# Optimization experiments

Measured on AMD Instinct MI355X. Metric: run time of the kernel, lower is better.

The kernel has to match this reference:

```python
import jax, jax.numpy as jnp
import numpy as np

DIM = 192; HEADS = 6; WS = 8; SHIFT = 4; HID = int(DIM * 4.0)
CAB_SCALE = 0.01; COMPRESS = 3; SQUEEZE = 30
B = 8; H0 = 128; W0 = 128


def window_partition(x, ws):
    Bn, H, W, C = x.shape
    x = x.reshape(Bn, H // ws, ws, W // ws, ws, C).transpose(0, 1, 3, 2, 4, 5)
    return x.reshape(-1, ws, ws, C)


def window_reverse(w, ws, H, W):
    Bn = w.shape[0] // ((H // ws) * (W // ws))
    x = w.reshape(Bn, H // ws, W // ws, ws, ws, -1).transpose(0, 1, 3, 2, 4, 5)
    return x.reshape(Bn, H, W, -1)


def layernorm(x, w, b):
    mu = jnp.mean(x, -1, keepdims=True)
    var = jnp.var(x, -1, keepdims=True)
    return (x - mu) * jax.lax.rsqrt(var + 1e-5) * w + b


def conv3x3(x, w, b):
    y = jax.lax.conv_general_dilated(x, w, (1, 1), [(1, 1), (1, 1)],
                                     dimension_numbers=('NCHW', 'OIHW', 'NCHW'))
    return y + b[None, :, None, None]


def _coords_table(ws):
    # continuous relative coords table, log-spaced as in SwinV2
    r = np.arange(-(ws - 1), ws, dtype=np.float32)
    t = np.stack(np.meshgrid(r, r, indexing='ij'), -1) / (ws - 1) * 8.0
    t = np.sign(t) * np.log2(np.abs(t) + 1.0) / np.log2(8.0)
    return jnp.asarray(t.reshape(-1, 2))  # ((2ws-1)^2, 2)


def _rel_index(ws):
    c = np.stack(np.meshgrid(np.arange(ws), np.arange(ws), indexing='ij')).reshape(2, -1)
    r = (c[:, :, None] - c[:, None, :]).transpose(1, 2, 0)
    r[..., 0] += ws - 1; r[..., 1] += ws - 1; r[..., 0] *= 2 * ws - 1
    return jnp.asarray(r.sum(-1))  # (N, N) int


def _attn_mask(H, W, ws, shift):
    img = np.zeros((1, H, W, 1), np.float32); cnt = 0
    for hs in (slice(0, -ws), slice(-ws, -shift), slice(-shift, None)):
        for wsl in (slice(0, -ws), slice(-ws, -shift), slice(-shift, None)):
            img[:, hs, wsl, :] = cnt; cnt += 1
    win = img.reshape(1, H // ws, ws, W // ws, ws, 1).transpose(0, 1, 3, 2, 4, 5).reshape(-1, ws * ws)
    m = win[:, None, :] - win[:, :, None]
    return jnp.asarray(np.where(m != 0, -100.0, 0.0).astype(np.float32))  # (nW, N, N)


def _forward(x, norm1_w, norm1_b, qkv_w, q_bias, v_bias, logit_scale,
             cpb_w1, cpb_b1, cpb_w2, proj_w, proj_b,
             cab1_w, cab1_b, cab2_w, cab2_b, ca1_w, ca1_b, ca2_w, ca2_b,
             norm2_w, norm2_b, fc1_w, fc1_b, fc2_w, fc2_b, H, W):
    Bn, L, C = x.shape
    nh = HEADS; hd = C // nh; N = WS * WS
    shortcut = x
    xn = layernorm(x, norm1_w, norm1_b)
    xi = xn.reshape(Bn, H, W, C)

    # ---- CAB branch (Conv-GELU-Conv + channel attention) ----
    xc = xi.transpose(0, 3, 1, 2)                      # NCHW
    c = conv3x3(xc, cab1_w, cab1_b)
    c = jax.nn.gelu(c, approximate=False)
    c = conv3x3(c, cab2_w, cab2_b)
    s = c.mean((2, 3))                                 # (B, C) squeeze
    s = jax.nn.relu(s @ ca1_w.T + ca1_b)
    s = jax.nn.sigmoid(s @ ca2_w.T + ca2_b)
    conv_x = (c * s[:, :, None, None]).transpose(0, 2, 3, 1).reshape(Bn, L, C)

    # ---- shifted-window cosine attention ----
    xs = jnp.roll(xi, (-SHIFT, -SHIFT), axis=(1, 2)) if SHIFT > 0 else xi
    xw = window_partition(xs, WS).reshape(-1, N, C)    # (B*nW, N, C)
    qkv_bias = jnp.concatenate([q_bias, jnp.zeros_like(v_bias), v_bias])
    qkv = (xw @ qkv_w.T + qkv_bias).reshape(-1, N, 3, nh, hd).transpose(2, 0, 3, 1, 4)
    q, k, v = qkv[0], qkv[1], qkv[2]                   # (B_, nh, N, hd)
    qn = q / jnp.maximum(jnp.linalg.norm(q, axis=-1, keepdims=True), 1e-12)
    kn = k / jnp.maximum(jnp.linalg.norm(k, axis=-1, keepdims=True), 1e-12)
    attn = jnp.einsum('bhnd,bhmd->bhnm', qn, kn)
    scale = jnp.exp(jnp.minimum(logit_scale, jnp.log(100.0)))  # (nh,1,1)
    attn = attn * scale
    # CPB MLP relative position bias
    hbias = jax.nn.relu(_coords_table(WS) @ cpb_w1.T + cpb_b1) @ cpb_w2.T  # (T, nh)
    rpb = hbias[_rel_index(WS).reshape(-1)].reshape(N, N, nh).transpose(2, 0, 1)
    attn = attn + 16.0 * jax.nn.sigmoid(rpb)[None]
    if SHIFT > 0:
        mask = _attn_mask(H, W, WS, SHIFT)             # (nW, N, N)
        nW = mask.shape[0]
        attn = (attn.reshape(-1, nW, nh, N, N) + mask[None, :, None]).reshape(-1, nh, N, N)
    attn = jax.nn.softmax(attn, axis=-1)
    out = jnp.einsum('bhnm,bhmd->bhnd', attn, v).transpose(0, 2, 1, 3).reshape(-1, N, C)
    out = out @ proj_w.T + proj_b
    out = window_reverse(out.reshape(-1, WS, WS, C), WS, H, W)
    if SHIFT > 0:
        out = jnp.roll(out, (SHIFT, SHIFT), axis=(1, 2))
    attn_x = out.reshape(Bn, L, C)

    x = shortcut + attn_x + CAB_SCALE * conv_x
    h = layernorm(x, norm2_w, norm2_b)
    h = jax.nn.gelu(h @ fc1_w.T + fc1_b, approximate=False) @ fc2_w.T + fc2_b
    return x + h


def setup_inputs() -> dict:
    key = jax.random.key(0)
    ks = jax.random.split(key, 24)
    r = lambda k, shp, s=0.02: (jax.random.normal(k, shp, jnp.float32) * s)
    C = DIM; Cc = DIM // COMPRESS; Cs = DIM // SQUEEZE
    return {
        'x': jax.random.normal(ks[0], (B, H0 * W0, C), jnp.float32),
        'H': H0, 'W': W0,
        'norm1_w': jnp.ones((C,), jnp.float32), 'norm1_b': jnp.zeros((C,), jnp.float32),
        'qkv_w': r(ks[1], (3 * C, C)),
        'q_bias': jnp.zeros((C,), jnp.float32), 'v_bias': jnp.zeros((C,), jnp.float32),
        'logit_scale': jnp.full((HEADS, 1, 1), np.log(10.0), jnp.float32),
        'cpb_w1': r(ks[2], (512, 2), 0.1), 'cpb_b1': jnp.zeros((512,), jnp.float32),
        'cpb_w2': r(ks[3], (HEADS, 512), 0.1),
        'proj_w': r(ks[4], (C, C)), 'proj_b': jnp.zeros((C,), jnp.float32),
        'cab1_w': r(ks[5], (Cc, C, 3, 3)), 'cab1_b': jnp.zeros((Cc,), jnp.float32),
        'cab2_w': r(ks[6], (C, Cc, 3, 3)), 'cab2_b': jnp.zeros((C,), jnp.float32),
        'ca1_w': r(ks[7], (Cs, C)), 'ca1_b': jnp.zeros((Cs,), jnp.float32),
        'ca2_w': r(ks[8], (C, Cs)), 'ca2_b': jnp.zeros((C,), jnp.float32),
        'norm2_w': jnp.ones((C,), jnp.float32), 'norm2_b': jnp.zeros((C,), jnp.float32),
        'fc1_w': r(ks[9], (HID, C)), 'fc1_b': jnp.zeros((HID,), jnp.float32),
        'fc2_w': r(ks[10], (C, HID)), 'fc2_b': jnp.zeros((C,), jnp.float32),
    }


def reference(x, H, W, norm1_w, norm1_b, qkv_w, q_bias, v_bias, logit_scale,
              cpb_w1, cpb_b1, cpb_w2, proj_w, proj_b,
              cab1_w, cab1_b, cab2_w, cab2_b, ca1_w, ca1_b, ca2_w, ca2_b,
              norm2_w, norm2_b, fc1_w, fc1_b, fc2_w, fc2_b):
    return _forward(x, norm1_w, norm1_b, qkv_w, q_bias, v_bias, logit_scale,
                    cpb_w1, cpb_b1, cpb_w2, proj_w, proj_b,
                    cab1_w, cab1_b, cab2_w, cab2_b, ca1_w, ca1_b, ca2_w, ca2_b,
                    norm2_w, norm2_b, fc1_w, fc1_b, fc2_w, fc2_b, int(H), int(W))
```

## Files before the change

kernel.cpp:

```cpp
#include <hip/hip_runtime.h>
#include <math.h>


typedef unsigned short u16;
typedef __attribute__((ext_vector_type(8))) short short8;
typedef __attribute__((ext_vector_type(4))) float f32x4;

#define DI static __device__ __forceinline__

DI float b2f(u16 u){ union{unsigned u; float f;} v; v.u = ((unsigned)u)<<16; return v.f; }
DI u16 f2b(float f){ union{float f; unsigned u;} v; v.f = f; unsigned r = v.u + 0x7fffu + ((v.u>>16)&1u); return (u16)(r>>16); }
DI float gelu_f(float x){ return 0.5f*x*(1.0f+erff(x*0.7071067811865475f)); }

#define L_TOK 131072
#define C2PLANE (12582912L)

__global__ __launch_bounds__(256) void ln_k(const float* __restrict__ in,
    const float* __restrict__ w, const float* __restrict__ b, u16* __restrict__ out)
{
  const int row  = blockIdx.x*4 + (threadIdx.x>>6);
  const int lane = threadIdx.x & 63;
  const float* r = in + (long)row*192;
  float v0 = r[lane], v1 = r[lane+64], v2 = r[lane+128];
  float s = v0+v1+v2;
  #pragma unroll
  for (int m=1;m<64;m<<=1) s += __shfl_xor(s, m);
  float mu = s*(1.0f/192.0f);
  float d0=v0-mu, d1=v1-mu, d2=v2-mu;
  float q = d0*d0+d1*d1+d2*d2;
  #pragma unroll
  for (int m=1;m<64;m<<=1) q += __shfl_xor(q, m);
  float rstd = rsqrtf(q*(1.0f/192.0f)+1e-5f);
  u16* o = out + (long)row*192;
  o[lane]     = f2b(d0*rstd*w[lane]    +b[lane]);
  o[lane+64]  = f2b(d1*rstd*w[lane+64] +b[lane+64]);
  o[lane+128] = f2b(d2*rstd*w[lane+128]+b[lane+128]);
}

__global__ __launch_bounds__(256) void prep_k(
    const float* __restrict__ qkv_w, const float* __restrict__ q_bias,
    const float* __restrict__ v_bias, const float* __restrict__ proj_w,
    const float* __restrict__ fc1_w, const float* __restrict__ fc2_w,
    const float* __restrict__ cab1_w, const float* __restrict__ cab2_w,
    const float* __restrict__ lgs,
    float* __restrict__ qkvbias, u16* __restrict__ wqkv, u16* __restrict__ wproj,
    u16* __restrict__ wfc1, u16* __restrict__ wfc2, u16* __restrict__ wt1,
    u16* __restrict__ wt2, float* __restrict__ scale6)
{
  int o = blockIdx.x*256 + threadIdx.x;
  if (o < 576){ qkvbias[o] = (o<192)? q_bias[o] : ((o<384)? 0.f : v_bias[o-384]); return; }
  o -= 576;
  if (o < 110592){ wqkv[o] = f2b(qkv_w[o]); return; } o -= 110592;
  if (o < 36864){ wproj[o] = f2b(proj_w[o]); return; } o -= 36864;
  if (o < 147456){ wfc1[o] = f2b(fc1_w[o]); return; } o -= 147456;
  if (o < 147456){ wfc2[o] = f2b(fc2_w[o]); return; } o -= 147456;
  if (o < 110592){
    int s = o/12288, r = o%12288, oc = r/192, ic = r%192, kh = s/3, kw = s%3;
    wt1[o] = f2b(cab1_w[((oc*192+ic)*3+kh)*3+kw]); return; } o -= 110592;
  if (o < 110592){
    int s = o/12288, r = o%12288, oc = r/64, ic = r%64, kh = s/3, kw = s%3;
    wt2[o] = f2b(cab2_w[((oc*64+ic)*3+kh)*3+kw]); return; } o -= 110592;
  if (o < 6){ scale6[o] = expf(fminf(lgs[o], logf(100.f))); }
}

__global__ __launch_bounds__(256) void rpb_k(const float* __restrict__ w1,
    const float* __restrict__ b1, const float* __restrict__ w2, float* __restrict__ rpbL)
{
  __shared__ float hb[225*6];
  const int tid = threadIdx.x;
  if (tid < 225){
    int di = tid/15, dj = tid%15;
    float vi = (di-7)*(8.0f/7.0f), vj = (dj-7)*(8.0f/7.0f);
    float t0 = (vi==0.f)?0.f:copysignf(log2f(fabsf(vi)+1.f)*(1.f/3.f), vi);
    float t1 = (vj==0.f)?0.f:copysignf(log2f(fabsf(vj)+1.f)*(1.f/3.f), vj);
    float acc[6] = {0,0,0,0,0,0};
    for (int hd=0; hd<512; ++hd){
      float a = fmaxf(t0*w1[hd*2] + t1*w1[hd*2+1] + b1[hd], 0.f);
      #pragma unroll
      for (int h=0;h<6;++h) acc[h] += a*w2[h*512+hd];
    }
    #pragma unroll
    for (int h=0;h<6;++h) hb[tid*6+h] = acc[h];
  }
  __syncthreads();
  for (int o = tid; o < 24576; o += 256){
    int i = o&3, lane = (o>>2)&63, mK = (o>>8)&3, nQ = (o>>10)&3, h = o>>12;
    int q = nQ*16 + (lane&15), k = mK*16 + (lane>>4)*4 + i;
    int idx = ((q>>3)-(k>>3)+7)*15 + ((q&7)-(k&7)+7);
    rpbL[o] = 16.0f/(1.0f+expf(-hb[idx*6+h]));
  }
}

template<int EPI, int KK, int NN>
__global__ __launch_bounds__(256) void gemm4_k(
    const u16* __restrict__ A, const u16* __restrict__ W,
    const float* __restrict__ bias, const float* __restrict__ resx,
    const u16* __restrict__ c2in, const float* __restrict__ sgate,
    float* __restrict__ outf, u16* __restrict__ outb)
{
  constexpr int KC = KK/192;
  constexpr int NP = NN/64;
  __shared__ __align__(16) u16 As[128*200];
  __shared__ __align__(16) u16 Bs[64*200];
  const int tid = threadIdx.x, w = tid>>6, lane = tid&63;
  const int fr = lane&15, g = lane>>4;
  const int m0 = blockIdx.x*128;
  u16*   obuf = Bs;
  float* fbuf = (float*)Bs;

  #define STAGE_A(kc) { \
    _Pragma("unroll") \
    for (int i=0;i<12;++i){ const int id=tid+i*256, row=id/24, cc=id%24; \
      *(short8*)&As[row*200+cc*8] = \
        *(const short8*)(A + (long)(m0+row)*KK + (kc)*192 + cc*8); } }
  #define KLOOP(accr) { \
    _Pragma("unroll") \
    for (int ks=0; ks<6; ++ks){ \
      short8 af0 = *(const short8*)&As[(w*32+     fr)*200 + ks*32 + g*8]; \
      short8 af1 = *(const short8*)&As[(w*32+16+  fr)*200 + ks*32 + g*8]; \
      _Pragma("unroll") \
      for (int nr=0;nr<4;++nr){ \
        short8 bf = *(const short8*)&Bs[(nr*16+fr)*200 + ks*32 + g*8]; \
        accr[0][nr] = __builtin_amdgcn_mfma_f32_16x16x32_bf16(af0, bf, accr[0][nr], 0,0,0); \
        accr[1][nr] = __builtin_amdgcn_mfma_f32_16x16x32_bf16(af1, bf, accr[1][nr], 0,0,0); \
      } } }

  #define EPI_BF16(accr, n0) { \
    __syncthreads(); \
    _Pragma("unroll") \
    for (int mr=0;mr<2;++mr) \
      _Pragma("unroll") \
      for (int nr=0;nr<4;++nr){ \
        const float bc = bias[(n0)+nr*16+fr]; \
        _Pragma("unroll") \
        for (int i=0;i<4;++i){ \
          const int tok = w*32+mr*16+g*4+i; \
          float v = accr[mr][nr][i] + bc; \
          if (EPI==4) v = gelu_f(v); \
          obuf[tok*72 + nr*16+fr] = f2b(v); } } \
    __syncthreads(); \
    _Pragma("unroll") \
    for (int j=0;j<4;++j){ \
      const int idx = tid + j*256, tok = idx>>3, cc = idx&7; \
      *(short8*)(outb + (long)(m0+tok)*NN + (n0) + cc*8) = \
          *(const short8*)&obuf[tok*72 + cc*8]; } }

  #define EPI_F32(accr, n0) { \
    _Pragma("unroll") \
    for (int h=0;h<2;++h){ \
      __syncthreads(); \
      if ((w>>1)==h){ \
        _Pragma("unroll") \
        for (int mr=0;mr<2;++mr) \
          _Pragma("unroll") \
          for (int nr=0;nr<4;++nr){ \
            const float bc = bias[(n0)+nr*16+fr]; \
            _Pragma("unroll") \
            for (int i=0;i<4;++i){ \
              const int tok = (w&1)*32+mr*16+g*4+i; \
              fbuf[tok*68 + nr*16+fr] = accr[mr][nr][i] + bc; } } } \
      __syncthreads(); \
      _Pragma("unroll") \
      for (int j=0;j<4;++j){ \
        const int idx = tid + j*256, t = idx>>4, cc = idx&15; \
        const int tokg = m0 + h*64 + t, gc0 = (n0) + cc*4; \
        f32x4 v = *(const f32x4*)&fbuf[t*68 + cc*4]; \
        const long o = (long)tokg*NN + gc0; \
        if constexpr (EPI==3){ \
          const f32x4 r = *(const f32x4*)(resx + o); \
          const int pl = (gc0>=96); \
          const u16* cp = c2in + (long)pl*C2PLANE + (long)tokg*96 + (gc0 - pl*96); \
          const float* sg = sgate + (tokg>>14)*192 + gc0; \
          _Pragma("unroll") \
          for (int e=0;e<4;++e) v[e] += r[e] + 0.01f*b2f(cp[e])*sg[e]; \
        } else { \
          const f32x4 r = *(const f32x4*)(outf + o); \
          _Pragma("unroll") \
          for (int e=0;e<4;++e) v[e] += r[e]; \
        } \
        *(f32x4*)(outf + o) = v; } } }

  short8 breg[6];
  #define LOADB(p) { \
    _Pragma("unroll") \
    for (int i=0;i<6;++i){ const int id=tid+i*256, br=id/24, cc=id%24; \
      breg[i] = *(const short8*)(W + (long)((p)*64+br)*KK + cc*8); } }
  #define STOREB() { \
    _Pragma("unroll") \
    for (int i=0;i<6;++i){ const int id=tid+i*256, br=id/24, cc=id%24; \
      *(short8*)&Bs[br*200+cc*8] = breg[i]; } }

  if constexpr (KC == 1){
    STAGE_A(0);
    LOADB(0);
    for (int p=0; p<NP; ++p){
      __syncthreads();
      STOREB();
      __syncthreads();
      if (p+1 < NP) LOADB(p+1);
      f32x4 acc[2][4];
      #pragma unroll
      for (int a=0;a<2;++a)
        #pragma unroll
        for (int b=0;b<4;++b) acc[a][b] = (f32x4){0.f,0.f,0.f,0.f};
      KLOOP(acc);
      if constexpr (EPI==0 || EPI==4){ EPI_BF16(acc, p*64); }
      else                           { EPI_F32(acc, p*64); }
    }
  } else {
    f32x4 acc[NP][2][4];
    #pragma unroll
    for (int p=0;p<NP;++p)
      #pragma unroll
      for (int a=0;a<2;++a)
        #pragma unroll
        for (int b=0;b<4;++b) acc[p][a][b] = (f32x4){0.f,0.f,0.f,0.f};
    for (int kc=0; kc<KC; ++kc){
      __syncthreads();
      STAGE_A(kc);
      #pragma unroll
      for (int p=0;p<NP;++p){
        __syncthreads();
        #pragma unroll
        for (int i=0;i<6;++i){ const int id=tid+i*256, br=id/24, cc=id%24;
          *(short8*)&Bs[br*200+cc*8] =
            *(const short8*)(W + (long)(p*64+br)*KK + kc*192 + cc*8); }
        __syncthreads();
        KLOOP(acc[p]);
      }
    }
    #pragma unroll
    for (int p=0;p<NP;++p){ EPI_F32(acc[p], p*64); }
  }
  #undef STAGE_A
  #undef KLOOP
  #undef EPI_BF16
  #undef EPI_F32
  #undef LOADB
  #undef STOREB
}

template<int EPI, int CG, int IC, int OCT, int OCP, int NR, int TG>
__global__ __launch_bounds__(256, 2) void conv4_k(
    const u16* __restrict__ A, const u16* __restrict__ Wt,
    const float* __restrict__ bias, u16* __restrict__ outb,
    float* __restrict__ ssum)
{
  constexpr int NTG = 9/TG, S = CG*NTG;
  constexpr int WN = (TG*OCP*4 + 255)/256;
  __shared__ __align__(16) u16 Ah[4*130*36];
  __shared__ __align__(16) u16 Wl[TG*OCP*36];
  const int tid = threadIdx.x, w = tid>>6, lane = tid&63;
  const int fr = lane&15, g = lane>>4;
  const int b = blockIdx.x>>6, y0 = (blockIdx.x&63)*2;
  const int oc0 = blockIdx.y*OCP;
  const int wrow = w>>1, wcol = (w&1)*64;

  f32x4 acc[4][NR];
  #pragma unroll
  for (int a=0;a<4;++a)
    #pragma unroll
    for (int n=0;n<NR;++n) acc[a][n] = (f32x4){0.f,0.f,0.f,0.f};

  short8 hreg[8], wreg[WN];

  #define PRELOAD(s) { \
    const int cg_=(s)/NTG, tg_=(s)%NTG; \
    if (tg_==0){ \
      _Pragma("unroll") \
      for (int i=0;i<8;++i){ \
        const int id=tid+i*256, p=id>>9, x=(id>>2)&127, cc=id&3, y=y0+p-1; \
        short8 v={0,0,0,0,0,0,0,0}; \
        if ((unsigned)y<128u) \
          v = *(const short8*)(A + (long)((((b<<7)|y)<<7)|x)*IC + cg_*32 + cc*8); \
        hreg[i]=v; } } \
    _Pragma("unroll") \
    for (int i=0;i<WN;++i){ \
      const int id=tid+i*256; \
      if (id < TG*OCP*4){ \
        const int t=id/(OCP*4), r=id%(OCP*4), oc=r>>2, cc=r&3; \
        wreg[i] = *(const short8*)(Wt + \
            (long)((tg_*TG+t)*OCT + oc0 + oc)*IC + cg_*32 + cc*8); } } }

  #define STORE_STAGED(s) { \
    const int tg_=(s)%NTG; \
    if (tg_==0){ \
      _Pragma("unroll") \
      for (int i=0;i<8;++i){ \
        const int id=tid+i*256, p=id>>9, x=(id>>2)&127, cc=id&3; \
        *(short8*)&Ah[(p*130 + x + 1)*36 + cc*8] = hreg[i]; } \
      if (tid < 32){ \
        const int p=tid>>3, r=tid&7, col=(r>>2)?129:0, cc=r&3; \
        *(short8*)&Ah[(p*130 + col)*36 + cc*8] = (short8){0,0,0,0,0,0,0,0}; } } \
    _Pragma("unroll") \
    for (int i=0;i<WN;++i){ \
      const int id=tid+i*256; \
      if (id < TG*OCP*4){ \
        const int t=id/(OCP*4), r=id%(OCP*4), oc=r>>2, cc=r&3; \
        *(short8*)&Wl[(t*OCP+oc)*36 + cc*8] = wreg[i]; } } }

  #define COMPUTE(s) { \
    const int tg_=(s)%NTG; \
    _Pragma("unroll") \
    for (int t=0;t<TG;++t){ \
      const int tap=tg_*TG+t, dy=tap/3, dx=tap%3; \
      short8 bf[NR]; \
      _Pragma("unroll") \
      for (int nr=0;nr<NR;++nr) \
        bf[nr] = *(const short8*)&Wl[(t*OCP + nr*16 + fr)*36 + g*8]; \
      short8 af[4]; \
      _Pragma("unroll") \
      for (int mr=0;mr<4;++mr) \
        af[mr] = *(const short8*)&Ah[((wrow+dy)*130 + wcol + mr*16 + fr + dx)*36 + g*8]; \
      _Pragma("unroll") \
      for (int mr=0;mr<4;++mr) \
        _Pragma("unroll") \
        for (int nr=0;nr<NR;++nr) \
          acc[mr][nr] = __builtin_amdgcn_mfma_f32_16x16x32_bf16(af[mr], bf[nr], acc[mr][nr], 0,0,0); } }

  PRELOAD(0);
  for (int s=0; s<S; ++s){
    __syncthreads();
    STORE_STAGED(s);
    __syncthreads();
    if (s+1 < S) PRELOAD(s+1);
    COMPUTE(s);
  }
  #undef PRELOAD
  #undef STORE_STAGED
  #undef COMPUTE

  if constexpr (EPI==2){
    #pragma unroll
    for (int nr=0;nr<NR;++nr){
      const float bc = bias[oc0 + nr*16 + fr];
      float s = 0.f;
      #pragma unroll
      for (int mr=0;mr<4;++mr)
        #pragma unroll
        for (int i=0;i<4;++i) s += acc[mr][nr][i] + bc;
      s += __shfl_xor(s,16); s += __shfl_xor(s,32);
      if (lane < 16) atomicAdd(&ssum[b*192 + oc0 + nr*16 + lane], s);
    }
  }

  u16* ob = Ah;
  const long tb = (long)(((b<<7)|y0)<<7);
  __syncthreads();
  if constexpr (EPI==1){
    #pragma unroll
    for (int mr=0;mr<4;++mr)
      #pragma unroll
      for (int nr=0;nr<NR;++nr){
        const float bc = bias[nr*16 + fr];
        #pragma unroll
        for (int i=0;i<4;++i){
          const int tok = wrow*128 + wcol + mr*16 + g*4 + i;
          ob[tok*72 + nr*16+fr] = f2b(gelu_f(acc[mr][nr][i] + bc));
        }
      }
    __syncthreads();
    #pragma unroll
    for (int j=0;j<8;++j){
      const int idx = tid + j*256, tok = idx>>3, cc = idx&7;
      *(short8*)(outb + (tb+tok)*OCP + cc*8) = *(const short8*)&ob[tok*72 + cc*8];
    }
  } else {
    const long pbase = (long)blockIdx.y*C2PLANE;
    #pragma unroll
    for (int h=0;h<2;++h){
      if (h) __syncthreads();
      if (wrow == h){
        #pragma unroll
        for (int mr=0;mr<4;++mr)
          #pragma unroll
          for (int nr=0;nr<NR;++nr){
            const float bc = bias[oc0 + nr*16 + fr];
            #pragma unroll
            for (int i=0;i<4;++i){
              const int tok = wcol + mr*16 + g*4 + i;
              ob[tok*104 + nr*16+fr] = f2b(acc[mr][nr][i] + bc);
            }
          }
      }
      __syncthreads();
      #pragma unroll
      for (int j=0;j<6;++j){
        const int idx = tid + j*256, t = idx/12, cc = idx%12;
        *(short8*)(outb + pbase + (tb + h*128 + t)*96 + cc*8) =
            *(const short8*)&ob[t*104 + cc*8];
      }
    }
  }
}

__global__ __launch_bounds__(256) void se_k(const float* __restrict__ ssum,
    const float* __restrict__ ca1w, const float* __restrict__ ca1b,
    const float* __restrict__ ca2w, const float* __restrict__ ca2b,
    float* __restrict__ sgate)
{
  __shared__ float hid[48];
  const int tid = threadIdx.x;
  if (tid < 48){
    int b = tid/6, cs = tid%6;
    float a = ca1b[cs];
    for (int c=0;c<192;++c) a += ssum[b*192+c]*(1.f/16384.f)*ca1w[cs*192+c];
    hid[tid] = fmaxf(a, 0.f);
  }
  __syncthreads();
  for (int o = tid; o < 1536; o += 256){
    int b = o/192, c = o%192;
    float a = ca2b[c];
    #pragma unroll
    for (int cs=0;cs<6;++cs) a += hid[b*6+cs]*ca2w[c*6+cs];
    sgate[o] = 1.f/(1.f+expf(-a));
  }
}

__global__ __launch_bounds__(256) void attn_k(const u16* __restrict__ qkv,
    const float* __restrict__ rpbL, const float* __restrict__ scale6,
    u16* __restrict__ aout)
{
  __shared__ int  lidx_s[4][64];
  __shared__ char region_s[4][64];
  __shared__ __align__(16) u16 p_s[4][64*72];
  const int tid = threadIdx.x, w = tid>>6, lane = tid&63;
  const int task = blockIdx.x*4 + w;
  const int win = task/6, h = task - win*6;
  const int b = win>>8, wn = win&255, wy = wn>>4, wx = wn&15;
  {
    int i = lane>>3, j = lane&7;
    int hs = wy*8+i, ws = wx*8+j;
    lidx_s[w][lane] = (b<<14) | (((hs+4)&127)<<7) | ((ws+4)&127);
    int hb = hs<120?0:(hs<124?1:2), wb = ws<120?0:(ws<124?1:2);
    region_s[w][lane] = (char)(hb*3+wb);
  }
  __syncthreads();
  const int g = lane>>4, l15 = lane&15;
  const bool edge = (wy==15) || (wx==15);
  const float scl = scale6[h];
  const f32x4 zf = {0.f,0.f,0.f,0.f};

  short8 kf[4];
  #pragma unroll
  for (int mt=0; mt<4; ++mt){
    const long base = (long)lidx_s[w][mt*16+l15]*576 + 192 + h*32 + g*8;
    short8 r = *(const short8*)(qkv + base);
    float f[8]; float ss = 0.f;
    #pragma unroll
    for (int e=0;e<8;++e){ f[e] = b2f((u16)r[e]); ss += f[e]*f[e]; }
    ss += __shfl_xor(ss,16); ss += __shfl_xor(ss,32);
    const float inv = 1.0f/fmaxf(sqrtf(ss), 1e-12f);
    #pragma unroll
    for (int e=0;e<8;++e) kf[mt][e] = (short)f2b(f[e]*inv);
  }

  #pragma unroll
  for (int nt=0; nt<4; ++nt){
    short8 qf;
    {
      const long base = (long)lidx_s[w][nt*16+l15]*576 + h*32 + g*8;
      short8 r = *(const short8*)(qkv + base);
      float f[8]; float ss = 0.f;
      #pragma unroll
      for (int e=0;e<8;++e){ f[e] = b2f((u16)r[e]); ss += f[e]*f[e]; }
      ss += __shfl_xor(ss,16); ss += __shfl_xor(ss,32);
      const float inv = 1.0f/fmaxf(sqrtf(ss), 1e-12f);
      #pragma unroll
      for (int e=0;e<8;++e) qf[e] = (short)f2b(f[e]*inv);
    }
    f32x4 st[4];
    #pragma unroll
    for (int mt=0; mt<4; ++mt)
      st[mt] = __builtin_amdgcn_mfma_f32_16x16x32_bf16(kf[mt], qf, zf, 0, 0, 0);
    float lv[16];
    const float* rp = rpbL + ((h*4+nt)*4)*256 + lane*4;
    const int rq = edge ? region_s[w][nt*16+l15] : 0;
    #pragma unroll
    for (int mt=0; mt<4; ++mt){
      const f32x4 rb = *(const f32x4*)(rp + mt*256);
      #pragma unroll
      for (int i=0;i<4;++i){
        float v = st[mt][i]*scl + rb[i];
        if (edge && region_s[w][mt*16+g*4+i] != rq) v -= 100.0f;
        lv[mt*4+i] = v;
      }
    }
    float mx = lv[0];
    #pragma unroll
    for (int t=1;t<16;++t) mx = fmaxf(mx, lv[t]);
    mx = fmaxf(mx, __shfl_xor(mx,16)); mx = fmaxf(mx, __shfl_xor(mx,32));
    float sum = 0.f;
    #pragma unroll
    for (int t=0;t<16;++t){ lv[t] = __expf(lv[t]-mx); sum += lv[t]; }
    sum += __shfl_xor(sum,16); sum += __shfl_xor(sum,32);
    const float isum = 1.0f/sum;
    u16* pr = p_s[w] + (nt*16+l15)*72;
    #pragma unroll
    for (int mt=0; mt<4; ++mt){
      #pragma unroll
      for (int j=0;j<2;++j){
        unsigned lo = f2b(lv[mt*4+2*j]  *isum);
        unsigned hi = f2b(lv[mt*4+2*j+1]*isum);
        *(unsigned*)(pr + mt*16 + g*4 + 2*j) = lo | (hi<<16);
      }
    }
  }

  short8 vf[2][2];
  #pragma unroll
  for (int nd=0; nd<2; ++nd)
    #pragma unroll
    for (int kc=0; kc<2; ++kc)
      #pragma unroll
      for (int e=0;e<8;++e){
        const int tok = kc*32 + g*8 + e;
        vf[nd][kc][e] = (short)qkv[(long)lidx_s[w][tok]*576 + 384 + h*32 + nd*16 + l15];
      }

  __syncthreads();

  #pragma unroll
  for (int mt=0; mt<4; ++mt){
    const short8 a0 = *(const short8*)(p_s[w] + (mt*16+l15)*72 +      g*8);
    const short8 a1 = *(const short8*)(p_s[w] + (mt*16+l15)*72 + 32 + g*8);
    #pragma unroll
    for (int nd=0; nd<2; ++nd){
      f32x4 o = __builtin_amdgcn_mfma_f32_16x16x32_bf16(a0, vf[nd][0], zf, 0, 0, 0);
      o = __builtin_amdgcn_mfma_f32_16x16x32_bf16(a1, vf[nd][1], o, 0, 0, 0);
      #pragma unroll
      for (int i=0;i<4;++i){
        const int q = mt*16 + g*4 + i;
        aout[(long)lidx_s[w][q]*192 + h*32 + nd*16 + l15] = f2b(o[i]);
      }
    }
  }
}

extern "C" void kernel_launch(void* const* d_in, const int* in_sizes, int n_in,
                              void* d_out, int out_size, void* d_ws, size_t ws_size,
                              hipStream_t stream)
{
  const float* x     = (const float*)d_in[0];
  const float* n1w   = (const float*)d_in[3];
  const float* n1b   = (const float*)d_in[4];
  const float* qkvw  = (const float*)d_in[5];
  const float* qb    = (const float*)d_in[6];
  const float* vb    = (const float*)d_in[7];
  const float* lgs   = (const float*)d_in[8];
  const float* cpb1w = (const float*)d_in[9];
  const float* cpb1b = (const float*)d_in[10];
  const float* cpb2w = (const float*)d_in[11];
  const float* projw = (const float*)d_in[12];
  const float* projb = (const float*)d_in[13];
  const float* cab1w = (const float*)d_in[14];
  const float* cab1b = (const float*)d_in[15];
  const float* cab2w = (const float*)d_in[16];
  const float* cab2b = (const float*)d_in[17];
  const float* ca1w  = (const float*)d_in[18];
  const float* ca1b  = (const float*)d_in[19];
  const float* ca2w  = (const float*)d_in[20];
  const float* ca2b  = (const float*)d_in[21];
  const float* n2w   = (const float*)d_in[22];
  const float* n2b   = (const float*)d_in[23];
  const float* fc1w  = (const float*)d_in[24];
  const float* fc1b  = (const float*)d_in[25];
  const float* fc2w  = (const float*)d_in[26];
  const float* fc2b  = (const float*)d_in[27];
  float* dout = (float*)d_out;
  char* ws = (char*)d_ws;

  constexpr size_t OFF_XN  = 0;
  constexpr size_t OFF_G1  = 50331648;
  constexpr size_t OFF_C2  = 67108864;
  constexpr size_t OFF_AO  = 167772160;
  constexpr size_t OFF_QKV = 218103808;
  constexpr size_t OFF_X2N = OFF_QKV;
  constexpr size_t OFF_H1  = 0;
  constexpr size_t OFF_SM  = 369098752;

  u16*   xn      = (u16*)(ws + OFF_XN);
  u16*   g1      = (u16*)(ws + OFF_G1);
  u16*   c2      = (u16*)(ws + OFF_C2);
  u16*   ao      = (u16*)(ws + OFF_AO);
  u16*   qkvb    = (u16*)(ws + OFF_QKV);
  u16*   x2n     = (u16*)(ws + OFF_X2N);
  u16*   h1      = (u16*)(ws + OFF_H1);
  float* qkvbias = (float*)(ws + OFF_SM);
  float* scale6  = (float*)(ws + OFF_SM + 4096);
  float* ssum    = (float*)(ws + OFF_SM + 8192);
  float* sgate   = (float*)(ws + OFF_SM + 16384);
  float* rpbL    = (float*)(ws + OFF_SM + 24576);
  u16*   wqkv    = (u16*)(ws + OFF_SM + 131072);
  u16*   wproj   = (u16*)(ws + OFF_SM + 360448);
  u16*   wfc1    = (u16*)(ws + OFF_SM + 434176);
  u16*   wfc2    = (u16*)(ws + OFF_SM + 729088);
  u16*   wt1     = (u16*)(ws + OFF_SM + 1024000);
  u16*   wt2     = (u16*)(ws + OFF_SM + 1245184);

  prep_k<<<2595, 256, 0, stream>>>(qkvw, qb, vb, projw, fc1w, fc2w, cab1w, cab2w,
                                   lgs, qkvbias, wqkv, wproj, wfc1, wfc2, wt1, wt2, scale6);
  rpb_k<<<1, 256, 0, stream>>>(cpb1w, cpb1b, cpb2w, rpbL);
  ln_k<<<32768, 256, 0, stream>>>(x, n1w, n1b, xn);
  hipMemsetAsync(ssum, 0, 1536*4, stream);
  conv4_k<1,6,192,64,64,4,9><<<dim3(512,1), 256, 0, stream>>>(xn, wt1, cab1b, g1, nullptr);
  conv4_k<2,2,64,192,96,6,3><<<dim3(512,2), 256, 0, stream>>>(g1, wt2, cab2b, c2, ssum);
  se_k<<<1, 256, 0, stream>>>(ssum, ca1w, ca1b, ca2w, ca2b, sgate);
  gemm4_k<0,192,576><<<1024, 256, 0, stream>>>(xn, wqkv, qkvbias,
      nullptr, nullptr, nullptr, nullptr, qkvb);
  attn_k<<<3072, 256, 0, stream>>>(qkvb, rpbL, scale6, ao);
  gemm4_k<3,192,192><<<1024, 256, 0, stream>>>(ao, wproj, projb,
      x, c2, sgate, dout, nullptr);
  ln_k<<<32768, 256, 0, stream>>>(dout, n2w, n2b, x2n);
  gemm4_k<4,192,768><<<1024, 256, 0, stream>>>(x2n, wfc1, fc1b,
      nullptr, nullptr, nullptr, nullptr, h1);
  gemm4_k<5,768,192><<<1024, 256, 0, stream>>>(h1, wfc2, fc2b,
      nullptr, nullptr, nullptr, dout, nullptr);
}
```

Measured before the change: 715.6 us.

## Fuse LN2, fc1, GELU and fc2 into one MLP kernel; add dedicated proj kernel

The second LayerNorm, fc1 with GELU, and fc2 with the residual add now run in a single kernel per 64-token tile. The 768-wide hidden activation is staged in LDS chunk by chunk instead of being written to and read back from global memory, and the separate LN and GEMM launches go away. The projection GEMM gets its own 64-row kernel that reads weight fragments straight from global memory. The cost is fc2 weight fragments loaded from global (L2) on every chunk, and lower MFMA reuse per wave.

```diff
diff --git a/kernel.cpp b/kernel.cpp
--- a/kernel.cpp
+++ b/kernel.cpp
@@ -12,7 +12,6 @@
 DI u16 f2b(float f){ union{float f; unsigned u;} v; v.f = f; unsigned r = v.u + 0x7fffu + ((v.u>>16)&1u); return (u16)(r>>16); }
 DI float gelu_f(float x){ return 0.5f*x*(1.0f+erff(x*0.7071067811865475f)); }
 
-#define L_TOK 131072
 #define C2PLANE (12582912L)
 
 __global__ __launch_bounds__(256) void ln_k(const float* __restrict__ in,
@@ -94,91 +93,20 @@
 template<int EPI, int KK, int NN>
 __global__ __launch_bounds__(256) void gemm4_k(
     const u16* __restrict__ A, const u16* __restrict__ W,
-    const float* __restrict__ bias, const float* __restrict__ resx,
-    const u16* __restrict__ c2in, const float* __restrict__ sgate,
-    float* __restrict__ outf, u16* __restrict__ outb)
-{
-  constexpr int KC = KK/192;
+    const float* __restrict__ bias, u16* __restrict__ outb)
+{
   constexpr int NP = NN/64;
   __shared__ __align__(16) u16 As[128*200];
   __shared__ __align__(16) u16 Bs[64*200];
   const int tid = threadIdx.x, w = tid>>6, lane = tid&63;
   const int fr = lane&15, g = lane>>4;
   const int m0 = blockIdx.x*128;
-  u16*   obuf = Bs;
-  float* fbuf = (float*)Bs;
-
-  #define STAGE_A(kc) { \
-    _Pragma("unroll") \
-    for (int i=0;i<12;++i){ const int id=tid+i*256, row=id/24, cc=id%24; \
-      *(short8*)&As[row*200+cc*8] = \
-        *(const short8*)(A + (long)(m0+row)*KK + (kc)*192 + cc*8); } }
-  #define KLOOP(accr) { \
-    _Pragma("unroll") \
-    for (int ks=0; ks<6; ++ks){ \
-      short8 af0 = *(const short8*)&As[(w*32+     fr)*200 + ks*32 + g*8]; \
-      short8 af1 = *(const short8*)&As[(w*32+16+  fr)*200 + ks*32 + g*8]; \
-      _Pragma("unroll") \
-      for (int nr=0;nr<4;++nr){ \
-        short8 bf = *(const short8*)&Bs[(nr*16+fr)*200 + ks*32 + g*8]; \
-        accr[0][nr] = __builtin_amdgcn_mfma_f32_16x16x32_bf16(af0, bf, accr[0][nr], 0,0,0); \
-        accr[1][nr] = __builtin_amdgcn_mfma_f32_16x16x32_bf16(af1, bf, accr[1][nr], 0,0,0); \
-      } } }
-
-  #define EPI_BF16(accr, n0) { \
-    __syncthreads(); \
-    _Pragma("unroll") \
-    for (int mr=0;mr<2;++mr) \
-      _Pragma("unroll") \
-      for (int nr=0;nr<4;++nr){ \
-        const float bc = bias[(n0)+nr*16+fr]; \
-        _Pragma("unroll") \
-        for (int i=0;i<4;++i){ \
-          const int tok = w*32+mr*16+g*4+i; \
-          float v = accr[mr][nr][i] + bc; \
-          if (EPI==4) v = gelu_f(v); \
-          obuf[tok*72 + nr*16+fr] = f2b(v); } } \
-    __syncthreads(); \
-    _Pragma("unroll") \
-    for (int j=0;j<4;++j){ \
-      const int idx = tid + j*256, tok = idx>>3, cc = idx&7; \
-      *(short8*)(outb + (long)(m0+tok)*NN + (n0) + cc*8) = \
-          *(const short8*)&obuf[tok*72 + cc*8]; } }
-
-  #define EPI_F32(accr, n0) { \
-    _Pragma("unroll") \
-    for (int h=0;h<2;++h){ \
-      __syncthreads(); \
-      if ((w>>1)==h){ \
-        _Pragma("unroll") \
-        for (int mr=0;mr<2;++mr) \
-          _Pragma("unroll") \
-          for (int nr=0;nr<4;++nr){ \
-            const float bc = bias[(n0)+nr*16+fr]; \
-            _Pragma("unroll") \
-            for (int i=0;i<4;++i){ \
-              const int tok = (w&1)*32+mr*16+g*4+i; \
-              fbuf[tok*68 + nr*16+fr] = accr[mr][nr][i] + bc; } } } \
-      __syncthreads(); \
-      _Pragma("unroll") \
-      for (int j=0;j<4;++j){ \
-        const int idx = tid + j*256, t = idx>>4, cc = idx&15; \
-        const int tokg = m0 + h*64 + t, gc0 = (n0) + cc*4; \
-        f32x4 v = *(const f32x4*)&fbuf[t*68 + cc*4]; \
-        const long o = (long)tokg*NN + gc0; \
-        if constexpr (EPI==3){ \
-          const f32x4 r = *(const f32x4*)(resx + o); \
-          const int pl = (gc0>=96); \
-          const u16* cp = c2in + (long)pl*C2PLANE + (long)tokg*96 + (gc0 - pl*96); \
-          const float* sg = sgate + (tokg>>14)*192 + gc0; \
-          _Pragma("unroll") \
-          for (int e=0;e<4;++e) v[e] += r[e] + 0.01f*b2f(cp[e])*sg[e]; \
-        } else { \
-          const f32x4 r = *(const f32x4*)(outf + o); \
-          _Pragma("unroll") \
-          for (int e=0;e<4;++e) v[e] += r[e]; \
-        } \
-        *(f32x4*)(outf + o) = v; } } }
+  u16* obuf = Bs;
+
+  #pragma unroll
+  for (int i=0;i<12;++i){ const int id=tid+i*256, row=id/24, cc=id%24;
+    *(short8*)&As[row*200+cc*8] =
+      *(const short8*)(A + (long)(m0+row)*KK + cc*8); }
 
   short8 breg[6];
   #define LOADB(p) { \
@@ -190,54 +118,201 @@
     for (int i=0;i<6;++i){ const int id=tid+i*256, br=id/24, cc=id%24; \
       *(short8*)&Bs[br*200+cc*8] = breg[i]; } }
 
-  if constexpr (KC == 1){
-    STAGE_A(0);
-    LOADB(0);
-    for (int p=0; p<NP; ++p){
-      __syncthreads();
-      STOREB();
-      __syncthreads();
-      if (p+1 < NP) LOADB(p+1);
-      f32x4 acc[2][4];
-      #pragma unroll
-      for (int a=0;a<2;++a)
+  LOADB(0);
+  for (int p=0; p<NP; ++p){
+    __syncthreads();
+    STOREB();
+    __syncthreads();
+    if (p+1 < NP) LOADB(p+1);
+    f32x4 acc[2][4];
+    #pragma unroll
+    for (int a=0;a<2;++a)
+      #pragma unroll
+      for (int b=0;b<4;++b) acc[a][b] = (f32x4){0.f,0.f,0.f,0.f};
+    #pragma unroll
+    for (int ks=0; ks<6; ++ks){
+      short8 af0 = *(const short8*)&As[(w*32+   fr)*200 + ks*32 + g*8];
+      short8 af1 = *(const short8*)&As[(w*32+16+fr)*200 + ks*32 + g*8];
+      #pragma unroll
+      for (int nr=0;nr<4;++nr){
+        short8 bf = *(const short8*)&Bs[(nr*16+fr)*200 + ks*32 + g*8];
+        acc[0][nr] = __builtin_amdgcn_mfma_f32_16x16x32_bf16(af0, bf, acc[0][nr], 0,0,0);
+        acc[1][nr] = __builtin_amdgcn_mfma_f32_16x16x32_bf16(af1, bf, acc[1][nr], 0,0,0);
+      } }
+    __syncthreads();
+    #pragma unroll
+    for (int mr=0;mr<2;++mr)
+      #pragma unroll
+      for (int nr=0;nr<4;++nr){
+        const float bc = bias[p*64+nr*16+fr];
         #pragma unroll
-        for (int b=0;b<4;++b) acc[a][b] = (f32x4){0.f,0.f,0.f,0.f};
-      KLOOP(acc);
-      if constexpr (EPI==0 || EPI==4){ EPI_BF16(acc, p*64); }
-      else                           { EPI_F32(acc, p*64); }
-    }
-  } else {
-    f32x4 acc[NP][2][4];
-    #pragma unroll
-    for (int p=0;p<NP;++p)
-      #pragma unroll
-      for (int a=0;a<2;++a)
-        #pragma unroll
-        for (int b=0;b<4;++b) acc[p][a][b] = (f32x4){0.f,0.f,0.f,0.f};
-    for (int kc=0; kc<KC; ++kc){
-      __syncthreads();
-      STAGE_A(kc);
-      #pragma unroll
-      for (int p=0;p<NP;++p){
-        __syncthreads();
-        #pragma unroll
-        for (int i=0;i<6;++i){ const int id=tid+i*256, br=id/24, cc=id%24;
-          *(short8*)&Bs[br*200+cc*8] =
-            *(const short8*)(W + (long)(p*64+br)*KK + kc*192 + cc*8); }
-        __syncthreads();
-        KLOOP(acc[p]);
-      }
-    }
-    #pragma unroll
-    for (int p=0;p<NP;++p){ EPI_F32(acc[p], p*64); }
-  }
-  #undef STAGE_A
-  #undef KLOOP
-  #undef EPI_BF16
-  #undef EPI_F32
+        for (int i=0;i<4;++i){
+          const int tok = w*32+mr*16+g*4+i;
+          obuf[tok*72 + nr*16+fr] = f2b(acc[mr][nr][i] + bc); } }
+    __syncthreads();
+    #pragma unroll
+    for (int j=0;j<4;++j){
+      const int idx = tid + j*256, tok = idx>>3, cc = idx&7;
+      *(short8*)(outb + (long)(m0+tok)*NN + p*64 + cc*8) =
+          *(const short8*)&obuf[tok*72 + cc*8]; }
+  }
   #undef LOADB
   #undef STOREB
+}
+
+__global__ __launch_bounds__(256) void proj_k(
+    const u16* __restrict__ A, const u16* __restrict__ W,
+    const float* __restrict__ bias, const float* __restrict__ resx,
+    const u16* __restrict__ c2in, const float* __restrict__ sgate,
+    float* __restrict__ outf)
+{
+  __shared__ __align__(16) u16 As[64*200];
+  const int tid = threadIdx.x, w = tid>>6, lane = tid&63;
+  const int fr = lane&15, g = lane>>4;
+  const int m0 = blockIdx.x*64;
+
+  #pragma unroll
+  for (int i=0;i<6;++i){ const int id=tid+i*256, r=id/24, cc=id%24;
+    *(short8*)&As[r*200+cc*8] = *(const short8*)(A + (long)(m0+r)*192 + cc*8); }
+  __syncthreads();
+
+  f32x4 acc[12];
+  #pragma unroll
+  for (int n=0;n<12;++n) acc[n] = (f32x4){0.f,0.f,0.f,0.f};
+  #pragma unroll
+  for (int ks=0;ks<6;++ks){
+    const short8 af = *(const short8*)&As[(w*16+fr)*200 + ks*32 + g*8];
+    #pragma unroll
+    for (int nr=0;nr<12;++nr){
+      const short8 bf = *(const short8*)(W + (long)(nr*16+fr)*192 + ks*32 + g*8);
+      acc[nr] = __builtin_amdgcn_mfma_f32_16x16x32_bf16(af, bf, acc[nr], 0,0,0);
+    }
+  }
+
+  float* fbuf = (float*)As;
+  #pragma unroll
+  for (int ch=0;ch<2;++ch){
+    __syncthreads();
+    #pragma unroll
+    for (int nr=0;nr<6;++nr){
+      const float bc = bias[ch*96 + nr*16 + fr];
+      #pragma unroll
+      for (int i=0;i<4;++i)
+        fbuf[(w*16+g*4+i)*100 + nr*16+fr] = acc[ch*6+nr][i] + bc;
+    }
+    __syncthreads();
+    #pragma unroll
+    for (int j=0;j<6;++j){
+      const int idx = tid + j*256, t = idx/24, cc = idx%24;
+      const int tokg = m0 + t, gc0 = ch*96 + cc*4;
+      const long o = (long)tokg*192 + gc0;
+      f32x4 v = *(const f32x4*)&fbuf[t*100 + cc*4];
+      const f32x4 r = *(const f32x4*)(resx + o);
+      const u16* cp = c2in + (long)ch*C2PLANE + (long)tokg*96 + cc*4;
+      const float* sg = sgate + (tokg>>14)*192 + gc0;
+      #pragma unroll
+      for (int e=0;e<4;++e) v[e] += r[e] + 0.01f*b2f(cp[e])*sg[e];
+      *(f32x4*)(outf + o) = v;
+    }
+  }
+}
+
+__global__ __launch_bounds__(256) void mlp_k(
+    const float* __restrict__ xio,
+    const float* __restrict__ lw, const float* __restrict__ lb,
+    const u16* __restrict__ w1, const float* __restrict__ b1,
+    const u16* __restrict__ w2, const float* __restrict__ b2,
+    float* __restrict__ out)
+{
+  __shared__ __align__(16) u16 As[64*200];
+  __shared__ __align__(16) u16 Bw[64*200];
+  __shared__ __align__(16) u16 Hs[64*72];
+  const int tid = threadIdx.x, w = tid>>6, lane = tid&63;
+  const int fr = lane&15, g = lane>>4;
+  const int m0 = blockIdx.x*64;
+
+  for (int it=0; it<16; ++it){
+    const int rl = w*16 + it;
+    const float* r = xio + (long)(m0+rl)*192;
+    float v0 = r[lane], v1 = r[lane+64], v2 = r[lane+128];
+    float s = v0+v1+v2;
+    #pragma unroll
+    for (int m=1;m<64;m<<=1) s += __shfl_xor(s, m);
+    const float mu = s*(1.0f/192.0f);
+    const float d0=v0-mu, d1=v1-mu, d2=v2-mu;
+    float q = d0*d0+d1*d1+d2*d2;
+    #pragma unroll
+    for (int m=1;m<64;m<<=1) q += __shfl_xor(q, m);
+    const float rstd = rsqrtf(q*(1.0f/192.0f)+1e-5f);
+    As[rl*200+lane]     = f2b(d0*rstd*lw[lane]    +lb[lane]);
+    As[rl*200+lane+64]  = f2b(d1*rstd*lw[lane+64] +lb[lane+64]);
+    As[rl*200+lane+128] = f2b(d2*rstd*lw[lane+128]+lb[lane+128]);
+  }
+  __syncthreads();
+
+  f32x4 acc2[12];
+  #pragma unroll
+  for (int n=0;n<12;++n) acc2[n] = (f32x4){0.f,0.f,0.f,0.f};
+
+  for (int p=0; p<12; ++p){
+    __syncthreads();
+    #pragma unroll
+    for (int i=0;i<6;++i){ const int id=tid+i*256, br=id/24, cc=id%24;
+      *(short8*)&Bw[br*200+cc*8] = *(const short8*)(w1 + (long)(p*64+br)*192 + cc*8); }
+    __syncthreads();
+    f32x4 a1[4];
+    #pragma unroll
+    for (int n=0;n<4;++n) a1[n] = (f32x4){0.f,0.f,0.f,0.f};
+    #pragma unroll
+    for (int ks=0;ks<6;++ks){
+      const short8 af = *(const short8*)&As[(w*16+fr)*200 + ks*32 + g*8];
+      #pragma unroll
+      for (int nr=0;nr<4;++nr){
+        const short8 bf = *(const short8*)&Bw[(nr*16+fr)*200 + ks*32 + g*8];
+        a1[nr] = __builtin_amdgcn_mfma_f32_16x16x32_bf16(af, bf, a1[nr], 0,0,0);
+      }
+    }
+    #pragma unroll
+    for (int nr=0;nr<4;++nr){
+      const float bc = b1[p*64 + nr*16 + fr];
+      #pragma unroll
+      for (int i=0;i<4;++i)
+        Hs[(w*16+g*4+i)*72 + nr*16+fr] = f2b(gelu_f(a1[nr][i] + bc));
+    }
+    #pragma unroll
+    for (int ks2=0;ks2<2;++ks2){
+      const short8 ah = *(const short8*)&Hs[(w*16+fr)*72 + ks2*32 + g*8];
+      #pragma unroll
+      for (int nr2=0;nr2<12;++nr2){
+        const short8 bf = *(const short8*)(w2 + (long)(nr2*16+fr)*768 + p*64 + ks2*32 + g*8);
+        acc2[nr2] = __builtin_amdgcn_mfma_f32_16x16x32_bf16(ah, bf, acc2[nr2], 0,0,0);
+      }
+    }
+  }
+
+  float* fbuf = (float*)As;
+  #pragma unroll
+  for (int ch=0;ch<2;++ch){
+    __syncthreads();
+    #pragma unroll
+    for (int nr=0;nr<6;++nr){
+      const float bc = b2[ch*96 + nr*16 + fr];
+      #pragma unroll
+      for (int i=0;i<4;++i)
+        fbuf[(w*16+g*4+i)*100 + nr*16+fr] = acc2[ch*6+nr][i] + bc;
+    }
+    __syncthreads();
+    #pragma unroll
+    for (int j=0;j<6;++j){
+      const int idx = tid + j*256, t = idx/24, cc = idx%24;
+      const long o = (long)(m0+t)*192 + ch*96 + cc*4;
+      f32x4 v = *(const f32x4*)&fbuf[t*100 + cc*4];
+      const f32x4 r = *(const f32x4*)(xio + o);
+      #pragma unroll
+      for (int e=0;e<4;++e) v[e] += r[e];
+      *(f32x4*)(out + o) = v;
+    }
+  }
 }
 
 template<int EPI, int CG, int IC, int OCT, int OCP, int NR, int TG>
@@ -575,8 +650,6 @@
   constexpr size_t OFF_C2  = 67108864;
   constexpr size_t OFF_AO  = 167772160;
   constexpr size_t OFF_QKV = 218103808;
-  constexpr size_t OFF_X2N = OFF_QKV;
-  constexpr size_t OFF_H1  = 0;
   constexpr size_t OFF_SM  = 369098752;
 
   u16*   xn      = (u16*)(ws + OFF_XN);
@@ -584,8 +657,6 @@
   u16*   c2      = (u16*)(ws + OFF_C2);
   u16*   ao      = (u16*)(ws + OFF_AO);
   u16*   qkvb    = (u16*)(ws + OFF_QKV);
-  u16*   x2n     = (u16*)(ws + OFF_X2N);
-  u16*   h1      = (u16*)(ws + OFF_H1);
   float* qkvbias = (float*)(ws + OFF_SM);
   float* scale6  = (float*)(ws + OFF_SM + 4096);
   float* ssum    = (float*)(ws + OFF_SM + 8192);
@@ -606,14 +677,8 @@
   conv4_k<1,6,192,64,64,4,9><<<dim3(512,1), 256, 0, stream>>>(xn, wt1, cab1b, g1, nullptr);
   conv4_k<2,2,64,192,96,6,3><<<dim3(512,2), 256, 0, stream>>>(g1, wt2, cab2b, c2, ssum);
   se_k<<<1, 256, 0, stream>>>(ssum, ca1w, ca1b, ca2w, ca2b, sgate);
-  gemm4_k<0,192,576><<<1024, 256, 0, stream>>>(xn, wqkv, qkvbias,
-      nullptr, nullptr, nullptr, nullptr, qkvb);
+  gemm4_k<0,192,576><<<1024, 256, 0, stream>>>(xn, wqkv, qkvbias, qkvb);
   attn_k<<<3072, 256, 0, stream>>>(qkvb, rpbL, scale6, ao);
-  gemm4_k<3,192,192><<<1024, 256, 0, stream>>>(ao, wproj, projb,
-      x, c2, sgate, dout, nullptr);
-  ln_k<<<32768, 256, 0, stream>>>(dout, n2w, n2b, x2n);
-  gemm4_k<4,192,768><<<1024, 256, 0, stream>>>(x2n, wfc1, fc1b,
-      nullptr, nullptr, nullptr, nullptr, h1);
-  gemm4_k<5,768,192><<<1024, 256, 0, stream>>>(h1, wfc2, fc2b,
-      nullptr, nullptr, nullptr, dout, nullptr);
-}
+  proj_k<<<2048, 256, 0, stream>>>(ao, wproj, projb, x, c2, sgate, dout);
+  mlp_k<<<2048, 256, 0, stream>>>(dout, n2w, n2b, wfc1, fc1b, wfc2, fc2b, dout);
+}
```

Measured after the change: 833.1 us. 1.16x slower.
